# Kernel optimization log

Measured on AMD Instinct MI355X. Metric: run time of the kernel, lower is better.

## Reference

```python
import jax, jax.numpy as jnp
import numpy as np

C = 512
HSIZE = C // 4
D, H, W = 18, 24, 24
N = D * H * W


def setup_inputs() -> dict:
    key = jax.random.key(0)
    ks = jax.random.split(key, 6)
    features = jax.random.normal(ks[0], (1, C, D, H, W), dtype=jnp.float32)
    Wi = jax.random.normal(ks[1], (HSIZE, C), dtype=jnp.float32) * 0.02
    bi = jax.random.normal(ks[2], (HSIZE,), dtype=jnp.float32) * 0.02
    Wj = jax.random.normal(ks[3], (HSIZE, C), dtype=jnp.float32) * 0.02
    bj = jax.random.normal(ks[4], (HSIZE,), dtype=jnp.float32) * 0.02
    # attention_agregate: shape (head=1, 1), xavier-uniform in the original
    agg = jax.random.uniform(ks[5], (1, 1), dtype=jnp.float32, minval=-1.0, maxval=1.0)
    return {"features": features, "Wi": Wi, "bi": bi, "Wj": Wj, "bj": bj, "agg": agg}


def reference(features, Wi, bi, Wj, bj, agg):
    # features: [1, C, D, H, W]; 1x1x1 convs == channel-wise matmuls
    x = features.reshape(C, N)                      # [C, N]
    fi = (Wi @ x + bi[:, None]).T                   # [N, hsize]  (conv_i output, permuted)
    fj = Wj @ x + bj[:, None]                       # [hsize, N]  (conv_j output)
    fk = x.T                                        # [N, C]      (raw features, NOT conv_k)
    # original: attn = (fi @ fj) * agg / N ; out = attn @ fk
    # linear chain reassociated: fi @ (fj @ fk) * agg / N  (same math, no NxN intermediate)
    scale = agg[0, 0] / jnp.float32(N)
    out_flat = (fi @ (fj @ fk)) * scale             # [N, C]
    return features + out_flat.T.reshape(1, C, D, H, W)
```

## Files before the change

### kernel.cpp

```cpp
#include <hip/hip_runtime.h>
#include <hip/hip_bf16.h>

#define C_   512
#define HS   128
#define NN   10368

typedef __bf16 bf16x8 __attribute__((ext_vector_type(8)));
typedef float  f32x4  __attribute__((ext_vector_type(4)));

__global__ void k_cast_transpose(const float* __restrict__ x,
                                 __bf16* __restrict__ xb,
                                 __bf16* __restrict__ xbT) {
    __shared__ float tile[64][65];
    const int bc = blockIdx.x;
    const int bn = blockIdx.y;
    const int t  = threadIdx.x;
    const int tr = t >> 6;
    const int tn = t & 63;
    const int c0 = bc * 64, n0 = bn * 64;
    for (int i = 0; i < 16; i++) {
        int c = tr + i * 4;
        float v = x[(size_t)(c0 + c) * NN + n0 + tn];
        xb[(size_t)(c0 + c) * NN + n0 + tn] = (__bf16)v;
        tile[c][tn] = v;
    }
    __syncthreads();
    for (int i = 0; i < 16; i++) {
        int n = tr + i * 4;
        xbT[(size_t)(n0 + n) * C_ + c0 + tn] = (__bf16)tile[tn][n];
    }
}

__global__ void k_prep(const float* __restrict__ Wi, const float* __restrict__ Wj,
                       __bf16* __restrict__ Wib, __bf16* __restrict__ Wjb,
                       float* __restrict__ Mtf) {
    int i = blockIdx.x * 256 + threadIdx.x;
    if (i < 65536)        Wib[i] = (__bf16)Wi[i];
    else if (i < 131072)  Wjb[i - 65536] = (__bf16)Wj[i - 65536];
    else                  Mtf[i - 131072] = 0.f;
}

__global__ void k_gemm12(const __bf16* __restrict__ xbT,
                         const __bf16* __restrict__ Wib, const __bf16* __restrict__ Wjb,
                         const float* __restrict__ bi, const float* __restrict__ bj,
                         __bf16* __restrict__ fj, __bf16* __restrict__ finm) {
    const int w    = blockIdx.x * 4 + (threadIdx.x >> 6);
    const int lane = threadIdx.x & 63;
    const int l16  = lane & 15;
    const int q    = lane >> 4;
    if (w < 648) {
        const int h0 = (w & 3) * 32, n0 = (w >> 2) * 64;
        f32x4 acc[2][4] = {};
        for (int k = 0; k < 512; k += 32) {
            bf16x8 a[2], b[4];
            #pragma unroll
            for (int i = 0; i < 2; i++)
                a[i] = *(const bf16x8*)(Wjb + (h0 + 16 * i + l16) * 512 + k + q * 8);
            #pragma unroll
            for (int t = 0; t < 4; t++)
                b[t] = *(const bf16x8*)(xbT + (size_t)(n0 + 16 * t + l16) * 512 + k + q * 8);
            #pragma unroll
            for (int i = 0; i < 2; i++)
                #pragma unroll
                for (int t = 0; t < 4; t++)
                    acc[i][t] = __builtin_amdgcn_mfma_f32_16x16x32_bf16(a[i], b[t], acc[i][t], 0, 0, 0);
        }
        #pragma unroll
        for (int i = 0; i < 2; i++)
            #pragma unroll
            for (int t = 0; t < 4; t++)
                #pragma unroll
                for (int r = 0; r < 4; r++) {
                    int h = h0 + 16 * i + q * 4 + r;
                    int n = n0 + 16 * t + l16;
                    fj[(size_t)h * NN + n] = (__bf16)(acc[i][t][r] + bj[h]);
                }
    } else {
        const int w2 = w - 648;
        const int n0 = (w2 >> 2) * 64, h0 = (w2 & 3) * 32;
        f32x4 acc[4][2] = {};
        for (int k = 0; k < 512; k += 32) {
            bf16x8 a[4], b[2];
            #pragma unroll
            for (int i = 0; i < 4; i++)
                a[i] = *(const bf16x8*)(xbT + (size_t)(n0 + 16 * i + l16) * 512 + k + q * 8);
            #pragma unroll
            for (int t = 0; t < 2; t++)
                b[t] = *(const bf16x8*)(Wib + (h0 + 16 * t + l16) * 512 + k + q * 8);
            #pragma unroll
            for (int i = 0; i < 4; i++)
                #pragma unroll
                for (int t = 0; t < 2; t++)
                    acc[i][t] = __builtin_amdgcn_mfma_f32_16x16x32_bf16(a[i], b[t], acc[i][t], 0, 0, 0);
        }
        #pragma unroll
        for (int i = 0; i < 4; i++)
            #pragma unroll
            for (int t = 0; t < 2; t++)
                #pragma unroll
                for (int r = 0; r < 4; r++) {
                    int n = n0 + 16 * i + q * 4 + r;
                    int h = h0 + 16 * t + l16;
                    finm[(size_t)n * HS + h] = (__bf16)(acc[i][t][r] + bi[h]);
                }
    }
}

__global__ void k_gemm3(const __bf16* __restrict__ xb, const __bf16* __restrict__ fj,
                        float* __restrict__ Mtf) {
    const int w    = blockIdx.x * 4 + (threadIdx.x >> 6);
    const int lane = threadIdx.x & 63;
    const int l16  = lane & 15;
    const int q    = lane >> 4;
    const int tp = w & 63, chunk = w >> 6;
    const int c0 = (tp >> 2) * 32, h0 = (tp & 3) * 32;
    const int k0 = chunk * 18 * 32;
    f32x4 acc[2][2] = {};
    for (int s = 0; s < 18; s++) {
        int k = k0 + s * 32;
        bf16x8 a[2], b[2];
        #pragma unroll
        for (int i = 0; i < 2; i++)
            a[i] = *(const bf16x8*)(xb + (size_t)(c0 + 16 * i + l16) * NN + k + q * 8);
        #pragma unroll
        for (int t = 0; t < 2; t++)
            b[t] = *(const bf16x8*)(fj + (size_t)(h0 + 16 * t + l16) * NN + k + q * 8);
        #pragma unroll
        for (int i = 0; i < 2; i++)
            #pragma unroll
            for (int t = 0; t < 2; t++)
                acc[i][t] = __builtin_amdgcn_mfma_f32_16x16x32_bf16(a[i], b[t], acc[i][t], 0, 0, 0);
    }
    #pragma unroll
    for (int i = 0; i < 2; i++)
        #pragma unroll
        for (int t = 0; t < 2; t++)
            #pragma unroll
            for (int r = 0; r < 4; r++) {
                int c = c0 + 16 * i + q * 4 + r;
                int h = h0 + 16 * t + l16;
                atomicAdd(&Mtf[c * HS + h], acc[i][t][r]);
            }
}

__global__ void k_scale(const float* __restrict__ Mtf, const float* __restrict__ agg,
                        __bf16* __restrict__ Mtb) {
    int i = blockIdx.x * 256 + threadIdx.x;
    float scale = agg[0] / (float)NN;
    if (i < 65536) Mtb[i] = (__bf16)(Mtf[i] * scale);
}

__global__ void k_gemm4(const __bf16* __restrict__ Mtb, const __bf16* __restrict__ finm,
                        const float* __restrict__ feat, float* __restrict__ out) {
    const int w    = blockIdx.x * 4 + (threadIdx.x >> 6);
    const int lane = threadIdx.x & 63;
    const int l16  = lane & 15;
    const int q    = lane >> 4;
    const int c0 = (w & 15) * 32, n0 = (w >> 4) * 64;
    f32x4 acc[2][4] = {};
    for (int k = 0; k < 128; k += 32) {
        bf16x8 a[2], b[4];
        #pragma unroll
        for (int i = 0; i < 2; i++)
            a[i] = *(const bf16x8*)(Mtb + (c0 + 16 * i + l16) * 128 + k + q * 8);
        #pragma unroll
        for (int t = 0; t < 4; t++)
            b[t] = *(const bf16x8*)(finm + (size_t)(n0 + 16 * t + l16) * 128 + k + q * 8);
        #pragma unroll
        for (int i = 0; i < 2; i++)
            #pragma unroll
            for (int t = 0; t < 4; t++)
                acc[i][t] = __builtin_amdgcn_mfma_f32_16x16x32_bf16(a[i], b[t], acc[i][t], 0, 0, 0);
    }
    #pragma unroll
    for (int i = 0; i < 2; i++)
        #pragma unroll
        for (int t = 0; t < 4; t++)
            #pragma unroll
            for (int r = 0; r < 4; r++) {
                int c = c0 + 16 * i + q * 4 + r;
                int n = n0 + 16 * t + l16;
                size_t idx = (size_t)c * NN + n;
                out[idx] = feat[idx] + acc[i][t][r];
            }
}

extern "C" void kernel_launch(void* const* d_in, const int* in_sizes, int n_in,
                              void* d_out, int out_size, void* d_ws, size_t ws_size,
                              hipStream_t stream) {
    const float* feat = (const float*)d_in[0];
    const float* Wi   = (const float*)d_in[1];
    const float* bi   = (const float*)d_in[2];
    const float* Wj   = (const float*)d_in[3];
    const float* bj   = (const float*)d_in[4];
    const float* agg  = (const float*)d_in[5];
    float* out = (float*)d_out;

    char* ws = (char*)d_ws;
    __bf16* xb   = (__bf16*)(ws);
    __bf16* xbT  = (__bf16*)(ws + 10616832);
    __bf16* Wib  = (__bf16*)(ws + 21233664);
    __bf16* Wjb  = (__bf16*)(ws + 21364736);
    __bf16* fj   = (__bf16*)(ws + 21495808);
    __bf16* finm = (__bf16*)(ws + 24150016);
    float*  Mtf  = (float*) (ws + 26804224);
    __bf16* Mtb  = (__bf16*)(ws + 27066368);

    k_cast_transpose<<<dim3(8, 162), 256, 0, stream>>>(feat, xb, xbT);
    k_prep<<<768, 256, 0, stream>>>(Wi, Wj, Wib, Wjb, Mtf);
    k_gemm12<<<324, 256, 0, stream>>>(xbT, Wib, Wjb, bi, bj, fj, finm);
    k_gemm3<<<288, 256, 0, stream>>>(xb, fj, Mtf);
    k_scale<<<256, 256, 0, stream>>>(Mtf, agg, Mtb);
    k_gemm4<<<648, 256, 0, stream>>>(Mtb, finm, feat, out);
}
```

Before: 143.9 us.

## Fuse prep kernels and replace atomic split-K with partial-sum reduction in consumer

Merges the cast/transpose and weight-cast kernels into one launch and drops the zeroing of the accumulator. The fj·x^T reduction now writes four partial slabs using an in-block LDS reduction instead of global atomicAdd. The final GEMM sums the four partials, converts to bf16 on load, and applies the agg/N scale in its epilogue, which removes the separate scale kernel. This cuts two launches and atomic traffic, at the cost of redundant partial-sum reads in every block of the last GEMM.

```diff
diff --git a/kernel.cpp b/kernel.cpp
--- a/kernel.cpp
+++ b/kernel.cpp
@@ -8,36 +8,45 @@
 typedef __bf16 bf16x8 __attribute__((ext_vector_type(8)));
 typedef float  f32x4  __attribute__((ext_vector_type(4)));
 
-__global__ void k_cast_transpose(const float* __restrict__ x,
+__global__ void k_prep_transpose(const float* __restrict__ x,
+                                 const float* __restrict__ Wi,
+                                 const float* __restrict__ Wj,
                                  __bf16* __restrict__ xb,
-                                 __bf16* __restrict__ xbT) {
-    __shared__ float tile[64][65];
-    const int bc = blockIdx.x;
-    const int bn = blockIdx.y;
-    const int t  = threadIdx.x;
-    const int tr = t >> 6;
-    const int tn = t & 63;
-    const int c0 = bc * 64, n0 = bn * 64;
-    for (int i = 0; i < 16; i++) {
-        int c = tr + i * 4;
-        float v = x[(size_t)(c0 + c) * NN + n0 + tn];
-        xb[(size_t)(c0 + c) * NN + n0 + tn] = (__bf16)v;
-        tile[c][tn] = v;
-    }
-    __syncthreads();
-    for (int i = 0; i < 16; i++) {
-        int n = tr + i * 4;
-        xbT[(size_t)(n0 + n) * C_ + c0 + tn] = (__bf16)tile[tn][n];
-    }
-}
-
-__global__ void k_prep(const float* __restrict__ Wi, const float* __restrict__ Wj,
-                       __bf16* __restrict__ Wib, __bf16* __restrict__ Wjb,
-                       float* __restrict__ Mtf) {
-    int i = blockIdx.x * 256 + threadIdx.x;
-    if (i < 65536)        Wib[i] = (__bf16)Wi[i];
-    else if (i < 131072)  Wjb[i - 65536] = (__bf16)Wj[i - 65536];
-    else                  Mtf[i - 131072] = 0.f;
+                                 __bf16* __restrict__ xbT,
+                                 __bf16* __restrict__ Wib,
+                                 __bf16* __restrict__ Wjb) {
+    const int b = blockIdx.x;
+    const int t = threadIdx.x;
+    if (b < 1296) {
+        __shared__ float tile[64][65];
+        const int bc = b & 7;
+        const int bn = b >> 3;
+        const int tr = t >> 6;
+        const int tn = t & 63;
+        const int c0 = bc * 64, n0 = bn * 64;
+        for (int i = 0; i < 16; i++) {
+            int c = tr + i * 4;
+            float v = x[(size_t)(c0 + c) * NN + n0 + tn];
+            xb[(size_t)(c0 + c) * NN + n0 + tn] = (__bf16)v;
+            tile[c][tn] = v;
+        }
+        __syncthreads();
+        for (int i = 0; i < 16; i++) {
+            int n = tr + i * 4;
+            xbT[(size_t)(n0 + n) * C_ + c0 + tn] = (__bf16)tile[tn][n];
+        }
+    } else {
+        const int b2 = b - 1296;
+        const float* src = (b2 < 32) ? Wi : Wj;
+        __bf16* dst      = (b2 < 32) ? Wib : Wjb;
+        const int off = (b2 & 31) * 2048 + t * 8;
+        float4 v0 = *(const float4*)(src + off);
+        float4 v1 = *(const float4*)(src + off + 4);
+        __bf16 o[8];
+        o[0] = (__bf16)v0.x; o[1] = (__bf16)v0.y; o[2] = (__bf16)v0.z; o[3] = (__bf16)v0.w;
+        o[4] = (__bf16)v1.x; o[5] = (__bf16)v1.y; o[6] = (__bf16)v1.z; o[7] = (__bf16)v1.w;
+        *(bf16x8*)(dst + off) = *(bf16x8*)o;
+    }
 }
 
 __global__ void k_gemm12(const __bf16* __restrict__ xbT,
@@ -106,66 +115,93 @@
     }
 }
 
-__global__ void k_gemm3(const __bf16* __restrict__ xb, const __bf16* __restrict__ fj,
-                        float* __restrict__ Mtf) {
-    const int w    = blockIdx.x * 4 + (threadIdx.x >> 6);
+__global__ void k_gemm3p(const __bf16* __restrict__ xb, const __bf16* __restrict__ fj,
+                         float* __restrict__ Mp) {
+    __shared__ float red[3][64][16];
+    const int b    = blockIdx.x;
+    const int v    = threadIdx.x >> 6;
     const int lane = threadIdx.x & 63;
     const int l16  = lane & 15;
     const int q    = lane >> 4;
-    const int tp = w & 63, chunk = w >> 6;
-    const int c0 = (tp >> 2) * 32, h0 = (tp & 3) * 32;
-    const int k0 = chunk * 18 * 32;
+    const int tile = b & 63, g = b >> 6;
+    const int c0 = (tile >> 2) * 32, h0 = (tile & 3) * 32;
+    const int chunk = g * 4 + v;
+    const int s0 = (chunk * 324) >> 4;
+    const int s1 = ((chunk + 1) * 324) >> 4;
     f32x4 acc[2][2] = {};
-    for (int s = 0; s < 18; s++) {
-        int k = k0 + s * 32;
-        bf16x8 a[2], b[2];
+    for (int s = s0; s < s1; s++) {
+        int k = s * 32;
+        bf16x8 a[2], bb[2];
         #pragma unroll
         for (int i = 0; i < 2; i++)
             a[i] = *(const bf16x8*)(xb + (size_t)(c0 + 16 * i + l16) * NN + k + q * 8);
         #pragma unroll
         for (int t = 0; t < 2; t++)
-            b[t] = *(const bf16x8*)(fj + (size_t)(h0 + 16 * t + l16) * NN + k + q * 8);
-        #pragma unroll
-        for (int i = 0; i < 2; i++)
-            #pragma unroll
-            for (int t = 0; t < 2; t++)
-                acc[i][t] = __builtin_amdgcn_mfma_f32_16x16x32_bf16(a[i], b[t], acc[i][t], 0, 0, 0);
-    }
-    #pragma unroll
-    for (int i = 0; i < 2; i++)
-        #pragma unroll
-        for (int t = 0; t < 2; t++)
-            #pragma unroll
-            for (int r = 0; r < 4; r++) {
-                int c = c0 + 16 * i + q * 4 + r;
-                int h = h0 + 16 * t + l16;
-                atomicAdd(&Mtf[c * HS + h], acc[i][t][r]);
-            }
-}
-
-__global__ void k_scale(const float* __restrict__ Mtf, const float* __restrict__ agg,
-                        __bf16* __restrict__ Mtb) {
-    int i = blockIdx.x * 256 + threadIdx.x;
-    float scale = agg[0] / (float)NN;
-    if (i < 65536) Mtb[i] = (__bf16)(Mtf[i] * scale);
-}
-
-__global__ void k_gemm4(const __bf16* __restrict__ Mtb, const __bf16* __restrict__ finm,
-                        const float* __restrict__ feat, float* __restrict__ out) {
+            bb[t] = *(const bf16x8*)(fj + (size_t)(h0 + 16 * t + l16) * NN + k + q * 8);
+        #pragma unroll
+        for (int i = 0; i < 2; i++)
+            #pragma unroll
+            for (int t = 0; t < 2; t++)
+                acc[i][t] = __builtin_amdgcn_mfma_f32_16x16x32_bf16(a[i], bb[t], acc[i][t], 0, 0, 0);
+    }
+    if (v > 0) {
+        #pragma unroll
+        for (int i = 0; i < 2; i++)
+            #pragma unroll
+            for (int t = 0; t < 2; t++)
+                #pragma unroll
+                for (int r = 0; r < 4; r++)
+                    red[v - 1][lane][i * 8 + t * 4 + r] = acc[i][t][r];
+    }
+    __syncthreads();
+    if (v == 0) {
+        float* dst = Mp + g * (C_ * HS);
+        #pragma unroll
+        for (int i = 0; i < 2; i++)
+            #pragma unroll
+            for (int t = 0; t < 2; t++)
+                #pragma unroll
+                for (int r = 0; r < 4; r++) {
+                    int j = i * 8 + t * 4 + r;
+                    float s = acc[i][t][r] + red[0][lane][j] + red[1][lane][j] + red[2][lane][j];
+                    int c = c0 + 16 * i + q * 4 + r;
+                    int h = h0 + 16 * t + l16;
+                    dst[c * HS + h] = s;
+                }
+    }
+}
+
+__global__ void k_gemm4(const float* __restrict__ Mp, const __bf16* __restrict__ finm,
+                        const float* __restrict__ feat, const float* __restrict__ agg,
+                        float* __restrict__ out) {
     const int w    = blockIdx.x * 4 + (threadIdx.x >> 6);
     const int lane = threadIdx.x & 63;
     const int l16  = lane & 15;
     const int q    = lane >> 4;
     const int c0 = (w & 15) * 32, n0 = (w >> 4) * 64;
+    const float scale = agg[0] * (1.0f / (float)NN);
     f32x4 acc[2][4] = {};
     for (int k = 0; k < 128; k += 32) {
         bf16x8 a[2], b[4];
         #pragma unroll
-        for (int i = 0; i < 2; i++)
-            a[i] = *(const bf16x8*)(Mtb + (c0 + 16 * i + l16) * 128 + k + q * 8);
+        for (int i = 0; i < 2; i++) {
+            const int base = (c0 + 16 * i + l16) * HS + k + q * 8;
+            f32x4 s0 = *(const f32x4*)(Mp + base);
+            f32x4 s1 = *(const f32x4*)(Mp + base + 4);
+            #pragma unroll
+            for (int g = 1; g < 4; g++) {
+                s0 += *(const f32x4*)(Mp + g * (C_ * HS) + base);
+                s1 += *(const f32x4*)(Mp + g * (C_ * HS) + base + 4);
+            }
+            #pragma unroll
+            for (int j = 0; j < 4; j++) {
+                a[i][j]     = (__bf16)s0[j];
+                a[i][4 + j] = (__bf16)s1[j];
+            }
+        }
         #pragma unroll
         for (int t = 0; t < 4; t++)
-            b[t] = *(const bf16x8*)(finm + (size_t)(n0 + 16 * t + l16) * 128 + k + q * 8);
+            b[t] = *(const bf16x8*)(finm + (size_t)(n0 + 16 * t + l16) * HS + k + q * 8);
         #pragma unroll
         for (int i = 0; i < 2; i++)
             #pragma unroll
@@ -181,7 +217,7 @@
                 int c = c0 + 16 * i + q * 4 + r;
                 int n = n0 + 16 * t + l16;
                 size_t idx = (size_t)c * NN + n;
-                out[idx] = feat[idx] + acc[i][t][r];
+                out[idx] = feat[idx] + scale * acc[i][t][r];
             }
 }
 
@@ -203,13 +239,10 @@
     __bf16* Wjb  = (__bf16*)(ws + 21364736);
     __bf16* fj   = (__bf16*)(ws + 21495808);
     __bf16* finm = (__bf16*)(ws + 24150016);
-    float*  Mtf  = (float*) (ws + 26804224);
-    __bf16* Mtb  = (__bf16*)(ws + 27066368);
-
-    k_cast_transpose<<<dim3(8, 162), 256, 0, stream>>>(feat, xb, xbT);
-    k_prep<<<768, 256, 0, stream>>>(Wi, Wj, Wib, Wjb, Mtf);
+    float*  Mp   = (float*) (ws + 26804224);
+
+    k_prep_transpose<<<1360, 256, 0, stream>>>(feat, Wi, Wj, xb, xbT, Wib, Wjb);
     k_gemm12<<<324, 256, 0, stream>>>(xbT, Wib, Wjb, bi, bj, fj, finm);
-    k_gemm3<<<288, 256, 0, stream>>>(xb, fj, Mtf);
-    k_scale<<<256, 256, 0, stream>>>(Mtf, agg, Mtb);
-    k_gemm4<<<648, 256, 0, stream>>>(Mtb, finm, feat, out);
-}
+    k_gemm3p<<<256, 256, 0, stream>>>(xb, fj, Mp);
+    k_gemm4<<<648, 256, 0, stream>>>(Mp, finm, feat, agg, out);
+}
```

New measurement: 151.6 us. 5.3% more time.

## Fuse all stages into one persistent cooperative kernel with grid syncs

Applied to the files above, without the earlier changes.

Replaces six separate kernel launches with a single cooperative kernel of 256 blocks x 512 threads that runs the cast/transpose, projection GEMMs, reduction GEMM and output GEMM as phases separated by grid.sync. The separate scale kernel is removed: the output GEMM converts the fp32 M matrix to bf16 in its loads and applies the agg/N scale in the epilogue. This targets launch overhead and inter-kernel gaps, at the cost of a grid of only 256 blocks, grid-wide barriers, and fixed-stride work loops that may leave parts of the GPU idle in some phases. If the cooperative launch fails it falls back to four phased launches.

```diff
diff --git a/kernel.cpp b/kernel.cpp
--- a/kernel.cpp
+++ b/kernel.cpp
@@ -1,188 +1,209 @@
 #include <hip/hip_runtime.h>
 #include <hip/hip_bf16.h>
+#include <hip/hip_cooperative_groups.h>
+
+namespace cg = cooperative_groups;
 
 #define C_   512
 #define HS   128
 #define NN   10368
 
 typedef __bf16 bf16x8 __attribute__((ext_vector_type(8)));
+typedef __bf16 bf16x4 __attribute__((ext_vector_type(4)));
 typedef float  f32x4  __attribute__((ext_vector_type(4)));
 
-__global__ void k_cast_transpose(const float* __restrict__ x,
-                                 __bf16* __restrict__ xb,
-                                 __bf16* __restrict__ xbT) {
+__global__ __launch_bounds__(512, 2) void k_fused(
+    const float* __restrict__ feat, const float* __restrict__ Wi,
+    const float* __restrict__ bi,   const float* __restrict__ Wj,
+    const float* __restrict__ bj,   const float* __restrict__ agg,
+    float* __restrict__ out,
+    __bf16* __restrict__ xb,  __bf16* __restrict__ xbT,
+    __bf16* __restrict__ Wib, __bf16* __restrict__ Wjb,
+    __bf16* __restrict__ fj,  __bf16* __restrict__ finm,
+    float* __restrict__ Mtf,  int phase)
+{
+    cg::grid_group grid = cg::this_grid();
     __shared__ float tile[64][65];
-    const int bc = blockIdx.x;
-    const int bn = blockIdx.y;
-    const int t  = threadIdx.x;
-    const int tr = t >> 6;
-    const int tn = t & 63;
-    const int c0 = bc * 64, n0 = bn * 64;
-    for (int i = 0; i < 16; i++) {
-        int c = tr + i * 4;
-        float v = x[(size_t)(c0 + c) * NN + n0 + tn];
-        xb[(size_t)(c0 + c) * NN + n0 + tn] = (__bf16)v;
-        tile[c][tn] = v;
-    }
-    __syncthreads();
-    for (int i = 0; i < 16; i++) {
-        int n = tr + i * 4;
-        xbT[(size_t)(n0 + n) * C_ + c0 + tn] = (__bf16)tile[tn][n];
-    }
-}
-
-__global__ void k_prep(const float* __restrict__ Wi, const float* __restrict__ Wj,
-                       __bf16* __restrict__ Wib, __bf16* __restrict__ Wjb,
-                       float* __restrict__ Mtf) {
-    int i = blockIdx.x * 256 + threadIdx.x;
-    if (i < 65536)        Wib[i] = (__bf16)Wi[i];
-    else if (i < 131072)  Wjb[i - 65536] = (__bf16)Wj[i - 65536];
-    else                  Mtf[i - 131072] = 0.f;
-}
-
-__global__ void k_gemm12(const __bf16* __restrict__ xbT,
-                         const __bf16* __restrict__ Wib, const __bf16* __restrict__ Wjb,
-                         const float* __restrict__ bi, const float* __restrict__ bj,
-                         __bf16* __restrict__ fj, __bf16* __restrict__ finm) {
-    const int w    = blockIdx.x * 4 + (threadIdx.x >> 6);
-    const int lane = threadIdx.x & 63;
+    const int t    = threadIdx.x;
+    const int gw   = blockIdx.x * 8 + (t >> 6);
+    const int lane = t & 63;
     const int l16  = lane & 15;
     const int q    = lane >> 4;
-    if (w < 648) {
-        const int h0 = (w & 3) * 32, n0 = (w >> 2) * 64;
-        f32x4 acc[2][4] = {};
-        for (int k = 0; k < 512; k += 32) {
-            bf16x8 a[2], b[4];
-            #pragma unroll
-            for (int i = 0; i < 2; i++)
-                a[i] = *(const bf16x8*)(Wjb + (h0 + 16 * i + l16) * 512 + k + q * 8);
-            #pragma unroll
-            for (int t = 0; t < 4; t++)
-                b[t] = *(const bf16x8*)(xbT + (size_t)(n0 + 16 * t + l16) * 512 + k + q * 8);
-            #pragma unroll
-            for (int i = 0; i < 2; i++)
-                #pragma unroll
-                for (int t = 0; t < 4; t++)
-                    acc[i][t] = __builtin_amdgcn_mfma_f32_16x16x32_bf16(a[i], b[t], acc[i][t], 0, 0, 0);
+
+    if (phase < 0 || phase == 0) {
+        for (int u = blockIdx.x; u < 1376; u += 256) {
+            if (u < 1296) {
+                const int c0 = (u & 7) * 64, n0 = (u >> 3) * 64;
+                const int tr = t >> 6, tn = t & 63;
+                #pragma unroll
+                for (int i = 0; i < 8; i++) {
+                    int c = tr + i * 8;
+                    float v = feat[(size_t)(c0 + c) * NN + n0 + tn];
+                    xb[(size_t)(c0 + c) * NN + n0 + tn] = (__bf16)v;
+                    tile[c][tn] = v;
+                }
+                __syncthreads();
+                #pragma unroll
+                for (int i = 0; i < 8; i++) {
+                    int n = tr + i * 8;
+                    xbT[(size_t)(n0 + n) * C_ + c0 + tn] = (__bf16)tile[tn][n];
+                }
+                __syncthreads();
+            } else if (u < 1360) {
+                const int b2 = u - 1296;
+                const float* src = (b2 < 32) ? Wi : Wj;
+                __bf16* dst      = (b2 < 32) ? Wib : Wjb;
+                const int off = (b2 & 31) * 2048 + t * 4;
+                float4 v = *(const float4*)(src + off);
+                bf16x4 o;
+                o[0] = (__bf16)v.x; o[1] = (__bf16)v.y;
+                o[2] = (__bf16)v.z; o[3] = (__bf16)v.w;
+                *(bf16x4*)(dst + off) = o;
+            } else {
+                const int j = u - 1360;
+                f32x4 z = {0.f, 0.f, 0.f, 0.f};
+                *(f32x4*)(Mtf + j * 4096 + t * 8)     = z;
+                *(f32x4*)(Mtf + j * 4096 + t * 8 + 4) = z;
+            }
+        }
+    }
+    if (phase < 0) grid.sync();
+
+    if (phase < 0 || phase == 1) {
+        const int w = gw;
+        if (w < 648) {
+            const int h0 = (w & 3) * 32, n0 = (w >> 2) * 64;
+            f32x4 acc[2][4] = {};
+            for (int k = 0; k < 512; k += 32) {
+                bf16x8 a[2], b[4];
+                #pragma unroll
+                for (int i = 0; i < 2; i++)
+                    a[i] = *(const bf16x8*)(Wjb + (h0 + 16 * i + l16) * 512 + k + q * 8);
+                #pragma unroll
+                for (int tt = 0; tt < 4; tt++)
+                    b[tt] = *(const bf16x8*)(xbT + (size_t)(n0 + 16 * tt + l16) * 512 + k + q * 8);
+                #pragma unroll
+                for (int i = 0; i < 2; i++)
+                    #pragma unroll
+                    for (int tt = 0; tt < 4; tt++)
+                        acc[i][tt] = __builtin_amdgcn_mfma_f32_16x16x32_bf16(a[i], b[tt], acc[i][tt], 0, 0, 0);
+            }
+            #pragma unroll
+            for (int i = 0; i < 2; i++)
+                #pragma unroll
+                for (int tt = 0; tt < 4; tt++)
+                    #pragma unroll
+                    for (int r = 0; r < 4; r++) {
+                        int h = h0 + 16 * i + q * 4 + r;
+                        int n = n0 + 16 * tt + l16;
+                        fj[(size_t)h * NN + n] = (__bf16)(acc[i][tt][r] + bj[h]);
+                    }
+        } else if (w < 1296) {
+            const int w2 = w - 648;
+            const int n0 = (w2 >> 2) * 64, h0 = (w2 & 3) * 32;
+            f32x4 acc[4][2] = {};
+            for (int k = 0; k < 512; k += 32) {
+                bf16x8 a[4], b[2];
+                #pragma unroll
+                for (int i = 0; i < 4; i++)
+                    a[i] = *(const bf16x8*)(xbT + (size_t)(n0 + 16 * i + l16) * 512 + k + q * 8);
+                #pragma unroll
+                for (int tt = 0; tt < 2; tt++)
+                    b[tt] = *(const bf16x8*)(Wib + (h0 + 16 * tt + l16) * 512 + k + q * 8);
+                #pragma unroll
+                for (int i = 0; i < 4; i++)
+                    #pragma unroll
+                    for (int tt = 0; tt < 2; tt++)
+                        acc[i][tt] = __builtin_amdgcn_mfma_f32_16x16x32_bf16(a[i], b[tt], acc[i][tt], 0, 0, 0);
+            }
+            #pragma unroll
+            for (int i = 0; i < 4; i++)
+                #pragma unroll
+                for (int tt = 0; tt < 2; tt++)
+                    #pragma unroll
+                    for (int r = 0; r < 4; r++) {
+                        int n = n0 + 16 * i + q * 4 + r;
+                        int h = h0 + 16 * tt + l16;
+                        finm[(size_t)n * HS + h] = (__bf16)(acc[i][tt][r] + bi[h]);
+                    }
+        }
+    }
+    if (phase < 0) grid.sync();
+
+    if (phase < 0 || phase == 2) {
+        const int tl = gw & 63, chunk = gw >> 6;
+        const int c0 = (tl >> 2) * 32, h0 = (tl & 3) * 32;
+        const int s0 = (chunk * 324) >> 5;
+        const int s1 = ((chunk + 1) * 324) >> 5;
+        f32x4 acc[2][2] = {};
+        for (int s = s0; s < s1; s++) {
+            int k = s * 32;
+            bf16x8 a[2], bb[2];
+            #pragma unroll
+            for (int i = 0; i < 2; i++)
+                a[i] = *(const bf16x8*)(xb + (size_t)(c0 + 16 * i + l16) * NN + k + q * 8);
+            #pragma unroll
+            for (int tt = 0; tt < 2; tt++)
+                bb[tt] = *(const bf16x8*)(fj + (size_t)(h0 + 16 * tt + l16) * NN + k + q * 8);
+            #pragma unroll
+            for (int i = 0; i < 2; i++)
+                #pragma unroll
+                for (int tt = 0; tt < 2; tt++)
+                    acc[i][tt] = __builtin_amdgcn_mfma_f32_16x16x32_bf16(a[i], bb[tt], acc[i][tt], 0, 0, 0);
         }
         #pragma unroll
         for (int i = 0; i < 2; i++)
             #pragma unroll
-            for (int t = 0; t < 4; t++)
+            for (int tt = 0; tt < 2; tt++)
                 #pragma unroll
                 for (int r = 0; r < 4; r++) {
-                    int h = h0 + 16 * i + q * 4 + r;
-                    int n = n0 + 16 * t + l16;
-                    fj[(size_t)h * NN + n] = (__bf16)(acc[i][t][r] + bj[h]);
-                }
-    } else {
-        const int w2 = w - 648;
-        const int n0 = (w2 >> 2) * 64, h0 = (w2 & 3) * 32;
-        f32x4 acc[4][2] = {};
-        for (int k = 0; k < 512; k += 32) {
-            bf16x8 a[4], b[2];
-            #pragma unroll
-            for (int i = 0; i < 4; i++)
-                a[i] = *(const bf16x8*)(xbT + (size_t)(n0 + 16 * i + l16) * 512 + k + q * 8);
-            #pragma unroll
-            for (int t = 0; t < 2; t++)
-                b[t] = *(const bf16x8*)(Wib + (h0 + 16 * t + l16) * 512 + k + q * 8);
-            #pragma unroll
-            for (int i = 0; i < 4; i++)
-                #pragma unroll
-                for (int t = 0; t < 2; t++)
-                    acc[i][t] = __builtin_amdgcn_mfma_f32_16x16x32_bf16(a[i], b[t], acc[i][t], 0, 0, 0);
-        }
-        #pragma unroll
-        for (int i = 0; i < 4; i++)
-            #pragma unroll
-            for (int t = 0; t < 2; t++)
-                #pragma unroll
-                for (int r = 0; r < 4; r++) {
-                    int n = n0 + 16 * i + q * 4 + r;
-                    int h = h0 + 16 * t + l16;
-                    finm[(size_t)n * HS + h] = (__bf16)(acc[i][t][r] + bi[h]);
-                }
-    }
-}
-
-__global__ void k_gemm3(const __bf16* __restrict__ xb, const __bf16* __restrict__ fj,
-                        float* __restrict__ Mtf) {
-    const int w    = blockIdx.x * 4 + (threadIdx.x >> 6);
-    const int lane = threadIdx.x & 63;
-    const int l16  = lane & 15;
-    const int q    = lane >> 4;
-    const int tp = w & 63, chunk = w >> 6;
-    const int c0 = (tp >> 2) * 32, h0 = (tp & 3) * 32;
-    const int k0 = chunk * 18 * 32;
-    f32x4 acc[2][2] = {};
-    for (int s = 0; s < 18; s++) {
-        int k = k0 + s * 32;
-        bf16x8 a[2], b[2];
-        #pragma unroll
-        for (int i = 0; i < 2; i++)
-            a[i] = *(const bf16x8*)(xb + (size_t)(c0 + 16 * i + l16) * NN + k + q * 8);
-        #pragma unroll
-        for (int t = 0; t < 2; t++)
-            b[t] = *(const bf16x8*)(fj + (size_t)(h0 + 16 * t + l16) * NN + k + q * 8);
-        #pragma unroll
-        for (int i = 0; i < 2; i++)
-            #pragma unroll
-            for (int t = 0; t < 2; t++)
-                acc[i][t] = __builtin_amdgcn_mfma_f32_16x16x32_bf16(a[i], b[t], acc[i][t], 0, 0, 0);
-    }
-    #pragma unroll
-    for (int i = 0; i < 2; i++)
-        #pragma unroll
-        for (int t = 0; t < 2; t++)
-            #pragma unroll
-            for (int r = 0; r < 4; r++) {
-                int c = c0 + 16 * i + q * 4 + r;
-                int h = h0 + 16 * t + l16;
-                atomicAdd(&Mtf[c * HS + h], acc[i][t][r]);
-            }
-}
-
-__global__ void k_scale(const float* __restrict__ Mtf, const float* __restrict__ agg,
-                        __bf16* __restrict__ Mtb) {
-    int i = blockIdx.x * 256 + threadIdx.x;
-    float scale = agg[0] / (float)NN;
-    if (i < 65536) Mtb[i] = (__bf16)(Mtf[i] * scale);
-}
-
-__global__ void k_gemm4(const __bf16* __restrict__ Mtb, const __bf16* __restrict__ finm,
-                        const float* __restrict__ feat, float* __restrict__ out) {
-    const int w    = blockIdx.x * 4 + (threadIdx.x >> 6);
-    const int lane = threadIdx.x & 63;
-    const int l16  = lane & 15;
-    const int q    = lane >> 4;
-    const int c0 = (w & 15) * 32, n0 = (w >> 4) * 64;
-    f32x4 acc[2][4] = {};
-    for (int k = 0; k < 128; k += 32) {
-        bf16x8 a[2], b[4];
-        #pragma unroll
-        for (int i = 0; i < 2; i++)
-            a[i] = *(const bf16x8*)(Mtb + (c0 + 16 * i + l16) * 128 + k + q * 8);
-        #pragma unroll
-        for (int t = 0; t < 4; t++)
-            b[t] = *(const bf16x8*)(finm + (size_t)(n0 + 16 * t + l16) * 128 + k + q * 8);
-        #pragma unroll
-        for (int i = 0; i < 2; i++)
-            #pragma unroll
-            for (int t = 0; t < 4; t++)
-                acc[i][t] = __builtin_amdgcn_mfma_f32_16x16x32_bf16(a[i], b[t], acc[i][t], 0, 0, 0);
-    }
-    #pragma unroll
-    for (int i = 0; i < 2; i++)
-        #pragma unroll
-        for (int t = 0; t < 4; t++)
-            #pragma unroll
-            for (int r = 0; r < 4; r++) {
-                int c = c0 + 16 * i + q * 4 + r;
-                int n = n0 + 16 * t + l16;
-                size_t idx = (size_t)c * NN + n;
-                out[idx] = feat[idx] + acc[i][t][r];
-            }
+                    int c = c0 + 16 * i + q * 4 + r;
+                    int h = h0 + 16 * tt + l16;
+                    atomicAdd(&Mtf[c * HS + h], acc[i][tt][r]);
+                }
+    }
+    if (phase < 0) grid.sync();
+
+    if (phase < 0 || phase == 3) {
+        const float scale = agg[0] * (1.0f / (float)NN);
+        for (int w = gw; w < 2592; w += 2048) {
+            const int c0 = (w & 15) * 32, n0 = (w >> 4) * 64;
+            f32x4 acc[2][4] = {};
+            for (int k = 0; k < 128; k += 32) {
+                bf16x8 a[2], b[4];
+                #pragma unroll
+                for (int i = 0; i < 2; i++) {
+                    const int base = (c0 + 16 * i + l16) * HS + k + q * 8;
+                    f32x4 s0 = *(const f32x4*)(Mtf + base);
+                    f32x4 s1 = *(const f32x4*)(Mtf + base + 4);
+                    #pragma unroll
+                    for (int j = 0; j < 4; j++) {
+                        a[i][j]     = (__bf16)s0[j];
+                        a[i][4 + j] = (__bf16)s1[j];
+                    }
+                }
+                #pragma unroll
+                for (int tt = 0; tt < 4; tt++)
+                    b[tt] = *(const bf16x8*)(finm + (size_t)(n0 + 16 * tt + l16) * HS + k + q * 8);
+                #pragma unroll
+                for (int i = 0; i < 2; i++)
+                    #pragma unroll
+                    for (int tt = 0; tt < 4; tt++)
+                        acc[i][tt] = __builtin_amdgcn_mfma_f32_16x16x32_bf16(a[i], b[tt], acc[i][tt], 0, 0, 0);
+            }
+            #pragma unroll
+            for (int i = 0; i < 2; i++)
+                #pragma unroll
+                for (int tt = 0; tt < 4; tt++)
+                    #pragma unroll
+                    for (int r = 0; r < 4; r++) {
+                        int c = c0 + 16 * i + q * 4 + r;
+                        int n = n0 + 16 * tt + l16;
+                        size_t idx = (size_t)c * NN + n;
+                        out[idx] = feat[idx] + scale * acc[i][tt][r];
+                    }
+        }
+    }
 }
 
 extern "C" void kernel_launch(void* const* d_in, const int* in_sizes, int n_in,
@@ -204,12 +225,23 @@
     __bf16* fj   = (__bf16*)(ws + 21495808);
     __bf16* finm = (__bf16*)(ws + 24150016);
     float*  Mtf  = (float*) (ws + 26804224);
-    __bf16* Mtb  = (__bf16*)(ws + 27066368);
-
-    k_cast_transpose<<<dim3(8, 162), 256, 0, stream>>>(feat, xb, xbT);
-    k_prep<<<768, 256, 0, stream>>>(Wi, Wj, Wib, Wjb, Mtf);
-    k_gemm12<<<324, 256, 0, stream>>>(xbT, Wib, Wjb, bi, bj, fj, finm);
-    k_gemm3<<<288, 256, 0, stream>>>(xb, fj, Mtf);
-    k_scale<<<256, 256, 0, stream>>>(Mtf, agg, Mtb);
-    k_gemm4<<<648, 256, 0, stream>>>(Mtb, finm, feat, out);
+
+    int phase_all = -1;
+    void* args[] = {
+        (void*)&feat, (void*)&Wi, (void*)&bi, (void*)&Wj, (void*)&bj, (void*)&agg,
+        (void*)&out, (void*)&xb, (void*)&xbT, (void*)&Wib, (void*)&Wjb,
+        (void*)&fj, (void*)&finm, (void*)&Mtf, (void*)&phase_all
+    };
+    hipError_t err = hipLaunchCooperativeKernel((void*)k_fused, dim3(256), dim3(512),
+                                                args, 0, stream);
+    if (err != hipSuccess) {
+        k_fused<<<256, 512, 0, stream>>>(feat, Wi, bi, Wj, bj, agg, out,
+                                         xb, xbT, Wib, Wjb, fj, finm, Mtf, 0);
+        k_fused<<<256, 512, 0, stream>>>(feat, Wi, bi, Wj, bj, agg, out,
+                                         xb, xbT, Wib, Wjb, fj, finm, Mtf, 1);
+        k_fused<<<256, 512, 0, stream>>>(feat, Wi, bi, Wj, bj, agg, out,
+                                         xb, xbT, Wib, Wjb, fj, finm, Mtf, 2);
+        k_fused<<<256, 512, 0, stream>>>(feat, Wi, bi, Wj, bj, agg, out,
+                                         xb, xbT, Wib, Wjb, fj, finm, Mtf, 3);
+    }
 }
```

Result: slower. 255.4 us (+77.5%).

## Fuse casts into GEMMs and replace atomic split-K with in-block reduction

Applied to the files above, without the earlier changes.

Drops the separate bf16 copy of features and the weight-cast/zeroing kernel, so the GEMMs now read fp32 features and weights directly and convert them to bf16 in registers. The fj·x^T reduction now uses 128 blocks of 8 waves that reduce their partial sums through shared memory, instead of fp32 atomics plus a separate scale kernel. The agg/N scale moves into the final GEMM epilogue. This cuts the pipeline from six launches to four and removes a 10 MB write, but the reduction GEMM now runs on only 128 blocks with one long serial K loop per wave, so it may not fill the GPU.

```diff
diff --git a/kernel.cpp b/kernel.cpp
--- a/kernel.cpp
+++ b/kernel.cpp
@@ -8,40 +8,35 @@
 typedef __bf16 bf16x8 __attribute__((ext_vector_type(8)));
 typedef float  f32x4  __attribute__((ext_vector_type(4)));
 
-__global__ void k_cast_transpose(const float* __restrict__ x,
-                                 __bf16* __restrict__ xb,
-                                 __bf16* __restrict__ xbT) {
+__global__ void k_transpose(const float* __restrict__ x, __bf16* __restrict__ xbT) {
     __shared__ float tile[64][65];
-    const int bc = blockIdx.x;
-    const int bn = blockIdx.y;
+    const int c0 = blockIdx.x * 64, n0 = blockIdx.y * 64;
     const int t  = threadIdx.x;
-    const int tr = t >> 6;
-    const int tn = t & 63;
-    const int c0 = bc * 64, n0 = bn * 64;
+    const int tr = t >> 6, tn = t & 63;
+    #pragma unroll
     for (int i = 0; i < 16; i++) {
         int c = tr + i * 4;
-        float v = x[(size_t)(c0 + c) * NN + n0 + tn];
-        xb[(size_t)(c0 + c) * NN + n0 + tn] = (__bf16)v;
-        tile[c][tn] = v;
+        tile[c][tn] = x[(size_t)(c0 + c) * NN + n0 + tn];
     }
     __syncthreads();
+    #pragma unroll
     for (int i = 0; i < 16; i++) {
         int n = tr + i * 4;
         xbT[(size_t)(n0 + n) * C_ + c0 + tn] = (__bf16)tile[tn][n];
     }
 }
 
-__global__ void k_prep(const float* __restrict__ Wi, const float* __restrict__ Wj,
-                       __bf16* __restrict__ Wib, __bf16* __restrict__ Wjb,
-                       float* __restrict__ Mtf) {
-    int i = blockIdx.x * 256 + threadIdx.x;
-    if (i < 65536)        Wib[i] = (__bf16)Wi[i];
-    else if (i < 131072)  Wjb[i - 65536] = (__bf16)Wj[i - 65536];
-    else                  Mtf[i - 131072] = 0.f;
+__device__ __forceinline__ bf16x8 load_f32x8_as_bf16(const float* __restrict__ p) {
+    float4 v0 = *(const float4*)p;
+    float4 v1 = *(const float4*)(p + 4);
+    bf16x8 o;
+    o[0] = (__bf16)v0.x; o[1] = (__bf16)v0.y; o[2] = (__bf16)v0.z; o[3] = (__bf16)v0.w;
+    o[4] = (__bf16)v1.x; o[5] = (__bf16)v1.y; o[6] = (__bf16)v1.z; o[7] = (__bf16)v1.w;
+    return o;
 }
 
 __global__ void k_gemm12(const __bf16* __restrict__ xbT,
-                         const __bf16* __restrict__ Wib, const __bf16* __restrict__ Wjb,
+                         const float* __restrict__ Wi, const float* __restrict__ Wj,
                          const float* __restrict__ bi, const float* __restrict__ bj,
                          __bf16* __restrict__ fj, __bf16* __restrict__ finm) {
     const int w    = blockIdx.x * 4 + (threadIdx.x >> 6);
@@ -55,25 +50,25 @@
             bf16x8 a[2], b[4];
             #pragma unroll
             for (int i = 0; i < 2; i++)
-                a[i] = *(const bf16x8*)(Wjb + (h0 + 16 * i + l16) * 512 + k + q * 8);
-            #pragma unroll
-            for (int t = 0; t < 4; t++)
-                b[t] = *(const bf16x8*)(xbT + (size_t)(n0 + 16 * t + l16) * 512 + k + q * 8);
+                a[i] = load_f32x8_as_bf16(Wj + (h0 + 16 * i + l16) * 512 + k + q * 8);
+            #pragma unroll
+            for (int tt = 0; tt < 4; tt++)
+                b[tt] = *(const bf16x8*)(xbT + (size_t)(n0 + 16 * tt + l16) * 512 + k + q * 8);
             #pragma unroll
             for (int i = 0; i < 2; i++)
                 #pragma unroll
-                for (int t = 0; t < 4; t++)
-                    acc[i][t] = __builtin_amdgcn_mfma_f32_16x16x32_bf16(a[i], b[t], acc[i][t], 0, 0, 0);
+                for (int tt = 0; tt < 4; tt++)
+                    acc[i][tt] = __builtin_amdgcn_mfma_f32_16x16x32_bf16(a[i], b[tt], acc[i][tt], 0, 0, 0);
         }
         #pragma unroll
         for (int i = 0; i < 2; i++)
             #pragma unroll
-            for (int t = 0; t < 4; t++)
+            for (int tt = 0; tt < 4; tt++)
                 #pragma unroll
                 for (int r = 0; r < 4; r++) {
                     int h = h0 + 16 * i + q * 4 + r;
-                    int n = n0 + 16 * t + l16;
-                    fj[(size_t)h * NN + n] = (__bf16)(acc[i][t][r] + bj[h]);
+                    int n = n0 + 16 * tt + l16;
+                    fj[(size_t)h * NN + n] = (__bf16)(acc[i][tt][r] + bj[h]);
                 }
     } else {
         const int w2 = w - 648;
@@ -85,103 +80,99 @@
             for (int i = 0; i < 4; i++)
                 a[i] = *(const bf16x8*)(xbT + (size_t)(n0 + 16 * i + l16) * 512 + k + q * 8);
             #pragma unroll
-            for (int t = 0; t < 2; t++)
-                b[t] = *(const bf16x8*)(Wib + (h0 + 16 * t + l16) * 512 + k + q * 8);
+            for (int tt = 0; tt < 2; tt++)
+                b[tt] = load_f32x8_as_bf16(Wi + (h0 + 16 * tt + l16) * 512 + k + q * 8);
             #pragma unroll
             for (int i = 0; i < 4; i++)
                 #pragma unroll
-                for (int t = 0; t < 2; t++)
-                    acc[i][t] = __builtin_amdgcn_mfma_f32_16x16x32_bf16(a[i], b[t], acc[i][t], 0, 0, 0);
+                for (int tt = 0; tt < 2; tt++)
+                    acc[i][tt] = __builtin_amdgcn_mfma_f32_16x16x32_bf16(a[i], b[tt], acc[i][tt], 0, 0, 0);
         }
         #pragma unroll
         for (int i = 0; i < 4; i++)
             #pragma unroll
-            for (int t = 0; t < 2; t++)
+            for (int tt = 0; tt < 2; tt++)
                 #pragma unroll
                 for (int r = 0; r < 4; r++) {
                     int n = n0 + 16 * i + q * 4 + r;
-                    int h = h0 + 16 * t + l16;
-                    finm[(size_t)n * HS + h] = (__bf16)(acc[i][t][r] + bi[h]);
+                    int h = h0 + 16 * tt + l16;
+                    finm[(size_t)n * HS + h] = (__bf16)(acc[i][tt][r] + bi[h]);
                 }
     }
 }
 
-__global__ void k_gemm3(const __bf16* __restrict__ xb, const __bf16* __restrict__ fj,
-                        float* __restrict__ Mtf) {
-    const int w    = blockIdx.x * 4 + (threadIdx.x >> 6);
-    const int lane = threadIdx.x & 63;
+__global__ void k_gemm3(const float* __restrict__ feat, const __bf16* __restrict__ fj,
+                        __bf16* __restrict__ Mtb) {
+    __shared__ float red[8][64][9];
+    const int b    = blockIdx.x;
+    const int t    = threadIdx.x;
+    const int wv   = t >> 6;
+    const int lane = t & 63;
     const int l16  = lane & 15;
     const int q    = lane >> 4;
-    const int tp = w & 63, chunk = w >> 6;
-    const int c0 = (tp >> 2) * 32, h0 = (tp & 3) * 32;
-    const int k0 = chunk * 18 * 32;
-    f32x4 acc[2][2] = {};
-    for (int s = 0; s < 18; s++) {
-        int k = k0 + s * 32;
-        bf16x8 a[2], b[2];
-        #pragma unroll
-        for (int i = 0; i < 2; i++)
-            a[i] = *(const bf16x8*)(xb + (size_t)(c0 + 16 * i + l16) * NN + k + q * 8);
-        #pragma unroll
-        for (int t = 0; t < 2; t++)
-            b[t] = *(const bf16x8*)(fj + (size_t)(h0 + 16 * t + l16) * NN + k + q * 8);
-        #pragma unroll
-        for (int i = 0; i < 2; i++)
-            #pragma unroll
-            for (int t = 0; t < 2; t++)
-                acc[i][t] = __builtin_amdgcn_mfma_f32_16x16x32_bf16(a[i], b[t], acc[i][t], 0, 0, 0);
-    }
-    #pragma unroll
-    for (int i = 0; i < 2; i++)
-        #pragma unroll
-        for (int t = 0; t < 2; t++)
-            #pragma unroll
-            for (int r = 0; r < 4; r++) {
-                int c = c0 + 16 * i + q * 4 + r;
-                int h = h0 + 16 * t + l16;
-                atomicAdd(&Mtf[c * HS + h], acc[i][t][r]);
-            }
-}
-
-__global__ void k_scale(const float* __restrict__ Mtf, const float* __restrict__ agg,
-                        __bf16* __restrict__ Mtb) {
-    int i = blockIdx.x * 256 + threadIdx.x;
-    float scale = agg[0] / (float)NN;
-    if (i < 65536) Mtb[i] = (__bf16)(Mtf[i] * scale);
+    const int c0 = (b >> 2) * 16, h0 = (b & 3) * 32;
+    const int s0 = (wv * 324) >> 3;
+    const int s1 = ((wv + 1) * 324) >> 3;
+    f32x4 acc[2] = {};
+    for (int s = s0; s < s1; s++) {
+        int k = s * 32;
+        bf16x8 a = load_f32x8_as_bf16(feat + (size_t)(c0 + l16) * NN + k + q * 8);
+        bf16x8 b0 = *(const bf16x8*)(fj + (size_t)(h0 + l16) * NN + k + q * 8);
+        bf16x8 b1 = *(const bf16x8*)(fj + (size_t)(h0 + 16 + l16) * NN + k + q * 8);
+        acc[0] = __builtin_amdgcn_mfma_f32_16x16x32_bf16(a, b0, acc[0], 0, 0, 0);
+        acc[1] = __builtin_amdgcn_mfma_f32_16x16x32_bf16(a, b1, acc[1], 0, 0, 0);
+    }
+    #pragma unroll
+    for (int tt = 0; tt < 2; tt++)
+        #pragma unroll
+        for (int r = 0; r < 4; r++)
+            red[wv][lane][tt * 4 + r] = acc[tt][r];
+    __syncthreads();
+    const int lane_e = t >> 3, j = t & 7;
+    float s = red[0][lane_e][j];
+    #pragma unroll
+    for (int v = 1; v < 8; v++) s += red[v][lane_e][j];
+    const int qe = lane_e >> 4, le = lane_e & 15;
+    const int tt = j >> 2, r = j & 3;
+    const int c = c0 + qe * 4 + r;
+    const int h = h0 + 16 * tt + le;
+    Mtb[c * HS + h] = (__bf16)s;
 }
 
 __global__ void k_gemm4(const __bf16* __restrict__ Mtb, const __bf16* __restrict__ finm,
-                        const float* __restrict__ feat, float* __restrict__ out) {
+                        const float* __restrict__ feat, const float* __restrict__ agg,
+                        float* __restrict__ out) {
     const int w    = blockIdx.x * 4 + (threadIdx.x >> 6);
     const int lane = threadIdx.x & 63;
     const int l16  = lane & 15;
     const int q    = lane >> 4;
     const int c0 = (w & 15) * 32, n0 = (w >> 4) * 64;
+    const float scale = agg[0] * (1.0f / (float)NN);
     f32x4 acc[2][4] = {};
     for (int k = 0; k < 128; k += 32) {
         bf16x8 a[2], b[4];
         #pragma unroll
         for (int i = 0; i < 2; i++)
-            a[i] = *(const bf16x8*)(Mtb + (c0 + 16 * i + l16) * 128 + k + q * 8);
-        #pragma unroll
-        for (int t = 0; t < 4; t++)
-            b[t] = *(const bf16x8*)(finm + (size_t)(n0 + 16 * t + l16) * 128 + k + q * 8);
+            a[i] = *(const bf16x8*)(Mtb + (c0 + 16 * i + l16) * HS + k + q * 8);
+        #pragma unroll
+        for (int tt = 0; tt < 4; tt++)
+            b[tt] = *(const bf16x8*)(finm + (size_t)(n0 + 16 * tt + l16) * HS + k + q * 8);
         #pragma unroll
         for (int i = 0; i < 2; i++)
             #pragma unroll
-            for (int t = 0; t < 4; t++)
-                acc[i][t] = __builtin_amdgcn_mfma_f32_16x16x32_bf16(a[i], b[t], acc[i][t], 0, 0, 0);
+            for (int tt = 0; tt < 4; tt++)
+                acc[i][tt] = __builtin_amdgcn_mfma_f32_16x16x32_bf16(a[i], b[tt], acc[i][tt], 0, 0, 0);
     }
     #pragma unroll
     for (int i = 0; i < 2; i++)
         #pragma unroll
-        for (int t = 0; t < 4; t++)
+        for (int tt = 0; tt < 4; tt++)
             #pragma unroll
             for (int r = 0; r < 4; r++) {
                 int c = c0 + 16 * i + q * 4 + r;
-                int n = n0 + 16 * t + l16;
+                int n = n0 + 16 * tt + l16;
                 size_t idx = (size_t)c * NN + n;
-                out[idx] = feat[idx] + acc[i][t][r];
+                out[idx] = feat[idx] + scale * acc[i][tt][r];
             }
 }
 
@@ -197,19 +188,13 @@
     float* out = (float*)d_out;
 
     char* ws = (char*)d_ws;
-    __bf16* xb   = (__bf16*)(ws);
-    __bf16* xbT  = (__bf16*)(ws + 10616832);
-    __bf16* Wib  = (__bf16*)(ws + 21233664);
-    __bf16* Wjb  = (__bf16*)(ws + 21364736);
-    __bf16* fj   = (__bf16*)(ws + 21495808);
-    __bf16* finm = (__bf16*)(ws + 24150016);
-    float*  Mtf  = (float*) (ws + 26804224);
-    __bf16* Mtb  = (__bf16*)(ws + 27066368);
-
-    k_cast_transpose<<<dim3(8, 162), 256, 0, stream>>>(feat, xb, xbT);
-    k_prep<<<768, 256, 0, stream>>>(Wi, Wj, Wib, Wjb, Mtf);
-    k_gemm12<<<324, 256, 0, stream>>>(xbT, Wib, Wjb, bi, bj, fj, finm);
-    k_gemm3<<<288, 256, 0, stream>>>(xb, fj, Mtf);
-    k_scale<<<256, 256, 0, stream>>>(Mtf, agg, Mtb);
-    k_gemm4<<<648, 256, 0, stream>>>(Mtb, finm, feat, out);
-}
+    __bf16* xbT  = (__bf16*)(ws);
+    __bf16* fj   = (__bf16*)(ws + 10616832);
+    __bf16* finm = (__bf16*)(ws + 13271040);
+    __bf16* Mtb  = (__bf16*)(ws + 15925248);
+
+    k_transpose<<<dim3(8, 162), 256, 0, stream>>>(feat, xbT);
+    k_gemm12<<<324, 256, 0, stream>>>(xbT, Wi, Wj, bi, bj, fj, finm);
+    k_gemm3<<<128, 512, 0, stream>>>(feat, fj, Mtb);
+    k_gemm4<<<648, 256, 0, stream>>>(Mtb, finm, feat, agg, out);
+}
```

New measurement: 168.7 us. 1.17x slower.
